# Optimization experiments

Measured on AMD Instinct MI355X. Metric: run time of the kernel, lower is better.

Reference implementation:

```python
import jax, jax.numpy as jnp
from jax import lax
import numpy as np

B, T, CIN, COUT, H = 8, 128, 64, 64, 256


def setup_inputs() -> dict:
    key = jax.random.key(0)
    ks = jax.random.split(key, 8)
    return {
        "x": jax.random.normal(ks[0], (B, T, CIN, H, 1), dtype=jnp.float32),
        "h0": jax.random.uniform(ks[1], (B, COUT, H, 1), dtype=jnp.float32),
        "c0": jax.random.uniform(ks[2], (B, COUT, H, 1), dtype=jnp.float32),
        "conv_w": jax.random.normal(ks[3], (4 * COUT, CIN + COUT, 3), dtype=jnp.float32) * 0.05,
        "conv_b": jax.random.normal(ks[4], (4 * COUT,), dtype=jnp.float32) * 0.05,
        "Wci": jax.random.normal(ks[5], (1, COUT, H, 1), dtype=jnp.float32) * 0.02,
        "Wcf": jax.random.normal(ks[6], (1, COUT, H, 1), dtype=jnp.float32) * 0.02,
        "Wco": jax.random.normal(ks[7], (1, COUT, H, 1), dtype=jnp.float32) * 0.02,
    }


def _convlstm_scan(x, h0, c0, conv_w, conv_b, Wci, Wcf, Wco):
    # drop trailing width-1 dim; work in [B, C, H]
    x3 = x[..., 0]            # [B, T, Cin, H]
    h = h0[..., 0]            # [B, Cout, H]
    c = c0[..., 0]
    wci, wcf, wco = Wci[..., 0], Wcf[..., 0], Wco[..., 0]  # [1, Cout, H]
    b = conv_b[None, :, None]

    def step(carry, xt):
        h, c = carry
        cat = jnp.concatenate([xt, h], axis=1)  # [B, Cin+Cout, H]
        conv = lax.conv_general_dilated(
            cat, conv_w, window_strides=(1,), padding="SAME",
            dimension_numbers=("NCH", "OIH", "NCH")) + b  # [B, 4*Cout, H]
        i, f, g, o = jnp.split(conv, 4, axis=1)
        i = jax.nn.sigmoid(i + wci * c)
        f = jax.nn.sigmoid(f + wcf * c)
        c_new = f * c + i * jnp.tanh(g)
        o = jax.nn.sigmoid(o + wco * c_new)
        h_new = o * jnp.tanh(c_new)
        return (h_new, c_new), (h_new, c_new)

    (_, _), (hs, cs) = lax.scan(step, (h, c), jnp.swapaxes(x3, 0, 1))
    # hs, cs: [T, B, Cout, H] -> [B, T, Cout, H, 1]
    hs = jnp.swapaxes(hs, 0, 1)[..., None]
    cs = jnp.swapaxes(cs, 0, 1)[..., None]
    return hs, cs


def reference(x, h0, c0, conv_w, conv_b, Wci, Wcf, Wco):
    return _convlstm_scan(x, h0, c0, conv_w, conv_b, Wci, Wcf, Wco)
```

## Files before the change

kernel.cpp:

```cpp
#include <hip/hip_runtime.h>


constexpr int Bn    = 8;
constexpr int Tn    = 128;
constexpr int CINn  = 64;
constexpr int COUTn = 64;
constexpr int Hn    = 256;
constexpr int ICAT  = CINn + COUTn;

constexpr int PT    = 64;
constexpr int WAVES = 4;
constexpr int COJ   = 2;
constexpr int CO_PER_BLOCK = WAVES * COJ;

__device__ __forceinline__ float sigmoidf_(float v) {
    return 1.0f / (1.0f + __expf(-v));
}

__global__ __launch_bounds__(256) void convlstm_step(
    const float* __restrict__ x,
    const float* __restrict__ h0,
    const float* __restrict__ c0,
    const float* __restrict__ w,
    const float* __restrict__ bias,
    const float* __restrict__ wci,
    const float* __restrict__ wcf,
    const float* __restrict__ wco,
    float* __restrict__ hs,
    float* __restrict__ cs,
    int t)
{
    const int lane = threadIdx.x & 63;
    const int wv   = __builtin_amdgcn_readfirstlane((int)(threadIdx.x >> 6));
    const int p    = blockIdx.x * PT + lane;
    const int b    = blockIdx.y;
    const int co0  = blockIdx.z * CO_PER_BLOCK + wv * COJ;

    const float* xt = x + (size_t)(b * Tn + t) * CINn * Hn;
    const float* hp = (t == 0) ? (h0 + (size_t)b * COUTn * Hn)
                               : (hs + (size_t)(b * Tn + (t - 1)) * COUTn * Hn);
    const float* cp = (t == 0) ? (c0 + (size_t)b * COUTn * Hn)
                               : (cs + (size_t)(b * Tn + (t - 1)) * COUTn * Hn);

    float acc[COJ][4];
#pragma unroll
    for (int j = 0; j < COJ; ++j)
#pragma unroll
        for (int g = 0; g < 4; ++g)
            acc[j][g] = bias[g * COUTn + co0 + j];

#pragma unroll 4
    for (int ic = 0; ic < CINn; ++ic) {
        const float* src = xt + (size_t)ic * Hn;
        const float v1 = src[p];
        const float v0 = (p > 0)      ? src[p - 1] : 0.0f;
        const float v2 = (p < Hn - 1) ? src[p + 1] : 0.0f;
        const float* wic = w + (size_t)ic * 3;
#pragma unroll
        for (int j = 0; j < COJ; ++j) {
#pragma unroll
            for (int g = 0; g < 4; ++g) {
                const float* wr =
                    wic + (size_t)(g * COUTn + co0 + j) * (ICAT * 3);
                acc[j][g] = fmaf(wr[0], v0,
                            fmaf(wr[1], v1,
                            fmaf(wr[2], v2, acc[j][g])));
            }
        }
    }

#pragma unroll 4
    for (int hc = 0; hc < COUTn; ++hc) {
        const float* src = hp + (size_t)hc * Hn;
        const float v1 = src[p];
        const float v0 = (p > 0)      ? src[p - 1] : 0.0f;
        const float v2 = (p < Hn - 1) ? src[p + 1] : 0.0f;
        const float* wic = w + (size_t)(CINn + hc) * 3;
#pragma unroll
        for (int j = 0; j < COJ; ++j) {
#pragma unroll
            for (int g = 0; g < 4; ++g) {
                const float* wr =
                    wic + (size_t)(g * COUTn + co0 + j) * (ICAT * 3);
                acc[j][g] = fmaf(wr[0], v0,
                            fmaf(wr[1], v1,
                            fmaf(wr[2], v2, acc[j][g])));
            }
        }
    }

#pragma unroll
    for (int j = 0; j < COJ; ++j) {
        const int co = co0 + j;
        const size_t cidx = (size_t)co * Hn + p;
        const float cprev = cp[cidx];
        const float iv = sigmoidf_(acc[j][0] + wci[cidx] * cprev);
        const float fv = sigmoidf_(acc[j][1] + wcf[cidx] * cprev);
        const float gv = tanhf(acc[j][2]);
        const float cn = fv * cprev + iv * gv;
        const float ov = sigmoidf_(acc[j][3] + wco[cidx] * cn);
        const float hn = ov * tanhf(cn);
        const size_t oidx = ((size_t)(b * Tn + t) * COUTn + co) * Hn + p;
        hs[oidx] = hn;
        cs[oidx] = cn;
    }
}

extern "C" void kernel_launch(void* const* d_in, const int* in_sizes, int n_in,
                              void* d_out, int out_size, void* d_ws, size_t ws_size,
                              hipStream_t stream) {
    (void)in_sizes; (void)n_in; (void)out_size; (void)d_ws; (void)ws_size;

    const float* x    = (const float*)d_in[0];
    const float* h0   = (const float*)d_in[1];
    const float* c0   = (const float*)d_in[2];
    const float* w    = (const float*)d_in[3];
    const float* bias = (const float*)d_in[4];
    const float* wci  = (const float*)d_in[5];
    const float* wcf  = (const float*)d_in[6];
    const float* wco  = (const float*)d_in[7];

    float* hs = (float*)d_out;
    float* cs = hs + (size_t)Bn * Tn * COUTn * Hn;

    dim3 grid(Hn / PT, Bn, COUTn / CO_PER_BLOCK);
    for (int t = 0; t < Tn; ++t) {
        convlstm_step<<<grid, 256, 0, stream>>>(
            x, h0, c0, w, bias, wci, wcf, wco, hs, cs, t);
    }
}
```

Measured before the change: 3.156 ms.

## Stage concatenated input tile in LDS and split gates across waves

Each block now loads the x/h input tile for 64 positions plus halo into swizzled shared memory once. Each wave then computes one gate type for 8 output channels using vectorized LDS reads. Gate results go through shared memory so the LSTM pointwise update can combine them. This removes redundant global loads of neighbouring positions at the cost of two barriers and extra LDS traffic.

```diff
diff --git a/kernel.cpp b/kernel.cpp
--- a/kernel.cpp
+++ b/kernel.cpp
@@ -7,11 +7,7 @@
 constexpr int COUTn = 64;
 constexpr int Hn    = 256;
 constexpr int ICAT  = CINn + COUTn;
-
-constexpr int PT    = 64;
-constexpr int WAVES = 4;
-constexpr int COJ   = 2;
-constexpr int CO_PER_BLOCK = WAVES * COJ;
+constexpr int PP    = 64;
 
 __device__ __forceinline__ float sigmoidf_(float v) {
     return 1.0f / (1.0f + __expf(-v));
@@ -21,7 +17,7 @@
     const float* __restrict__ x,
     const float* __restrict__ h0,
     const float* __restrict__ c0,
-    const float* __restrict__ w,
+    const float* __restrict__ wg,
     const float* __restrict__ bias,
     const float* __restrict__ wci,
     const float* __restrict__ wcf,
@@ -30,11 +26,15 @@
     float* __restrict__ cs,
     int t)
 {
-    const int lane = threadIdx.x & 63;
-    const int wv   = __builtin_amdgcn_readfirstlane((int)(threadIdx.x >> 6));
-    const int p    = blockIdx.x * PT + lane;
-    const int b    = blockIdx.y;
-    const int co0  = blockIdx.z * CO_PER_BLOCK + wv * COJ;
+    __shared__ float cat[66 * 128];
+    __shared__ float conv_out[32 * 64];
+
+    const int tid = threadIdx.x;
+    const int p_l = tid & 63;
+    const int icg = tid >> 6;
+    const int p0  = blockIdx.x * PP;
+    const int b   = blockIdx.y;
+    const int coz = blockIdx.z;
 
     const float* xt = x + (size_t)(b * Tn + t) * CINn * Hn;
     const float* hp = (t == 0) ? (h0 + (size_t)b * COUTn * Hn)
@@ -42,65 +42,104 @@
     const float* cp = (t == 0) ? (c0 + (size_t)b * COUTn * Hn)
                                : (cs + (size_t)(b * Tn + (t - 1)) * COUTn * Hn);
 
-    float acc[COJ][4];
+    {
+        float vals[32];
 #pragma unroll
-    for (int j = 0; j < COJ; ++j)
+        for (int icc = 0; icc < 32; ++icc) {
+            const int ic = icc * 4 + icg;
+            const float* src = (ic < CINn) ? (xt + (size_t)ic * Hn)
+                                           : (hp + (size_t)(ic - CINn) * Hn);
+            vals[icc] = src[p0 + p_l];
+        }
+        const int row = p_l + 1;
 #pragma unroll
-        for (int g = 0; g < 4; ++g)
-            acc[j][g] = bias[g * COUTn + co0 + j];
-
-#pragma unroll 4
-    for (int ic = 0; ic < CINn; ++ic) {
-        const float* src = xt + (size_t)ic * Hn;
-        const float v1 = src[p];
-        const float v0 = (p > 0)      ? src[p - 1] : 0.0f;
-        const float v2 = (p < Hn - 1) ? src[p + 1] : 0.0f;
-        const float* wic = w + (size_t)ic * 3;
-#pragma unroll
-        for (int j = 0; j < COJ; ++j) {
-#pragma unroll
-            for (int g = 0; g < 4; ++g) {
-                const float* wr =
-                    wic + (size_t)(g * COUTn + co0 + j) * (ICAT * 3);
-                acc[j][g] = fmaf(wr[0], v0,
-                            fmaf(wr[1], v1,
-                            fmaf(wr[2], v2, acc[j][g])));
+        for (int icc = 0; icc < 32; ++icc) {
+            const int ic   = icc * 4 + icg;
+            const int slot = (ic >> 2) ^ (row & 31);
+            cat[row * 128 + slot * 4 + (ic & 3)] = vals[icc];
+        }
+        if (tid < 128) {
+            const int ic = tid;
+            float v = 0.0f;
+            if (p0 > 0) {
+                const float* src = (ic < CINn) ? (xt + (size_t)ic * Hn)
+                                               : (hp + (size_t)(ic - CINn) * Hn);
+                v = src[p0 - 1];
             }
+            const int slot = (ic >> 2);
+            cat[slot * 4 + (ic & 3)] = v;
+        } else {
+            const int ic = tid - 128;
+            float v = 0.0f;
+            if (p0 + PP < Hn) {
+                const float* src = (ic < CINn) ? (xt + (size_t)ic * Hn)
+                                               : (hp + (size_t)(ic - CINn) * Hn);
+                v = src[p0 + PP];
+            }
+            const int slot = (ic >> 2) ^ (65 & 31);
+            cat[65 * 128 + slot * 4 + (ic & 3)] = v;
         }
     }
+    __syncthreads();
 
-#pragma unroll 4
-    for (int hc = 0; hc < COUTn; ++hc) {
-        const float* src = hp + (size_t)hc * Hn;
-        const float v1 = src[p];
-        const float v0 = (p > 0)      ? src[p - 1] : 0.0f;
-        const float v2 = (p < Hn - 1) ? src[p + 1] : 0.0f;
-        const float* wic = w + (size_t)(CINn + hc) * 3;
+    const int wv    = __builtin_amdgcn_readfirstlane(tid >> 6);
+    const int chan0 = wv * COUTn + coz * 8;
+    const float* wbase = wg + (size_t)chan0 * (ICAT * 3);
+
+    float acc[8];
 #pragma unroll
-        for (int j = 0; j < COJ; ++j) {
+    for (int k = 0; k < 8; ++k) acc[k] = bias[chan0 + k];
+
+    const float4* cat4 = (const float4*)cat;
+    const int r0 = p_l, r1 = p_l + 1, r2 = p_l + 2;
+    const int s0 = (r0 & 31), s1 = (r1 & 31), s2 = (r2 & 31);
+
+#pragma unroll 2
+    for (int icq = 0; icq < 32; ++icq) {
+        const float4 a0 = cat4[r0 * 32 + (icq ^ s0)];
+        const float4 a1 = cat4[r1 * 32 + (icq ^ s1)];
+        const float4 a2 = cat4[r2 * 32 + (icq ^ s2)];
+        const float in0[4] = {a0.x, a0.y, a0.z, a0.w};
+        const float in1[4] = {a1.x, a1.y, a1.z, a1.w};
+        const float in2[4] = {a2.x, a2.y, a2.z, a2.w};
 #pragma unroll
-            for (int g = 0; g < 4; ++g) {
-                const float* wr =
-                    wic + (size_t)(g * COUTn + co0 + j) * (ICAT * 3);
-                acc[j][g] = fmaf(wr[0], v0,
-                            fmaf(wr[1], v1,
-                            fmaf(wr[2], v2, acc[j][g])));
+        for (int k = 0; k < 8; ++k) {
+            const float* wr = wbase + (size_t)k * (ICAT * 3) + icq * 12;
+#pragma unroll
+            for (int i = 0; i < 4; ++i) {
+                acc[k] = fmaf(wr[3 * i + 0], in0[i],
+                          fmaf(wr[3 * i + 1], in1[i],
+                          fmaf(wr[3 * i + 2], in2[i], acc[k])));
             }
         }
     }
 
 #pragma unroll
-    for (int j = 0; j < COJ; ++j) {
-        const int co = co0 + j;
-        const size_t cidx = (size_t)co * Hn + p;
+    for (int k = 0; k < 8; ++k)
+        conv_out[(wv * 8 + k) * 64 + p_l] = acc[k];
+    __syncthreads();
+
+    const int c2 = tid >> 6;
+    const int pg = p0 + p_l;
+#pragma unroll
+    for (int j = 0; j < 2; ++j) {
+        const int co_l = c2 * 2 + j;
+        const int co   = coz * 8 + co_l;
+        const float pi = conv_out[(0 * 8 + co_l) * 64 + p_l];
+        const float pf = conv_out[(1 * 8 + co_l) * 64 + p_l];
+        const float pg_ = conv_out[(2 * 8 + co_l) * 64 + p_l];
+        const float po = conv_out[(3 * 8 + co_l) * 64 + p_l];
+
+        const size_t cidx = (size_t)co * Hn + pg;
         const float cprev = cp[cidx];
-        const float iv = sigmoidf_(acc[j][0] + wci[cidx] * cprev);
-        const float fv = sigmoidf_(acc[j][1] + wcf[cidx] * cprev);
-        const float gv = tanhf(acc[j][2]);
+        const float iv = sigmoidf_(pi + wci[cidx] * cprev);
+        const float fv = sigmoidf_(pf + wcf[cidx] * cprev);
+        const float gv = tanhf(pg_);
         const float cn = fv * cprev + iv * gv;
-        const float ov = sigmoidf_(acc[j][3] + wco[cidx] * cn);
+        const float ov = sigmoidf_(po + wco[cidx] * cn);
         const float hn = ov * tanhf(cn);
-        const size_t oidx = ((size_t)(b * Tn + t) * COUTn + co) * Hn + p;
+
+        const size_t oidx = ((size_t)(b * Tn + t) * COUTn + co) * Hn + pg;
         hs[oidx] = hn;
         cs[oidx] = cn;
     }
@@ -123,7 +162,7 @@
     float* hs = (float*)d_out;
     float* cs = hs + (size_t)Bn * Tn * COUTn * Hn;
 
-    dim3 grid(Hn / PT, Bn, COUTn / CO_PER_BLOCK);
+    dim3 grid(Hn / PP, Bn, 8);
     for (int t = 0; t < Tn; ++t) {
         convlstm_step<<<grid, 256, 0, stream>>>(
             x, h0, c0, w, bias, wci, wcf, wco, hs, cs, t);
```

Measured after the change: 2.853 ms. -9.6%, faster.
